# Optimization experiments

Measured on AMD Instinct MI355X. Metric: run time of the kernel, lower is better.

## Reference

```python
import jax, jax.numpy as jnp
import numpy as np
from jax import lax

NPOINT = 1024
NSAMPLE = 32
EPS = 1e-5


def setup_inputs() -> dict:
    key = jax.random.key(0)
    ks = jax.random.split(key, 8)
    B, N, CF = 16, 4096, 64
    xyz = jax.random.normal(ks[0], (B, N, 3), jnp.float32)
    points = jax.random.normal(ks[1], (B, N, CF), jnp.float32)
    in_ch = 3 + CF
    # 1x1 Conv2d weights stored as (out_ch, in_ch); kaiming-ish scale
    w0 = jax.random.normal(ks[2], (64, in_ch), jnp.float32) / np.sqrt(in_ch)
    w1 = jax.random.normal(ks[3], (64, 64), jnp.float32) / np.sqrt(64)
    w2 = jax.random.normal(ks[4], (128, 64), jnp.float32) / np.sqrt(64)
    z64 = jnp.zeros((64,), jnp.float32)
    z128 = jnp.zeros((128,), jnp.float32)
    o64 = jnp.ones((64,), jnp.float32)
    o128 = jnp.ones((128,), jnp.float32)
    return {
        "xyz": xyz, "points": points,
        "w0": w0, "b0": z64, "g0": o64, "bb0": z64,
        "w1": w1, "b1": z64, "g1": o64, "bb1": z64,
        "w2": w2, "b2": z128, "g2": o128, "bb2": z128,
    }


def _fps(xyz, npoint):
    """Iterative farthest point sampling. xyz: (B,N,3) -> (B,npoint) int32.
    Deterministic start at index 0 (torch uses a random start)."""
    B, N, _ = xyz.shape

    def step(carry, _):
        distance, farthest = carry
        centroid = jnp.take_along_axis(xyz, farthest[:, None, None], axis=1)  # (B,1,3)
        dist = jnp.sum((xyz - centroid) ** 2, -1)  # (B,N)
        distance = jnp.minimum(distance, dist)
        new_far = jnp.argmax(distance, axis=-1).astype(jnp.int32)
        return (distance, new_far), farthest

    init = (jnp.full((B, N), 1e10, xyz.dtype), jnp.zeros((B,), jnp.int32))
    _, cents = lax.scan(step, init, None, length=npoint)  # (npoint, B)
    return cents.T  # (B, npoint)


def _gather(pts, idx):
    """pts: (B,N,C), idx: (B,S,K) -> (B,S,K,C)"""
    return jax.vmap(lambda p, i: p[i])(pts, idx)


def _bn_relu(x, g, b):
    # training-mode BatchNorm over all axes except channel (last), biased var
    mean = jnp.mean(x, axis=(0, 1, 2))
    var = jnp.var(x, axis=(0, 1, 2))
    return jax.nn.relu(g * (x - mean) * lax.rsqrt(var + EPS) + b)


def reference(xyz, points, w0, b0, g0, bb0, w1, b1, g1, bb1, w2, b2, g2, bb2):
    B, N, _ = xyz.shape
    fps_idx = _fps(xyz, NPOINT)  # (B,S)
    new_xyz = jnp.take_along_axis(xyz, fps_idx[..., None], axis=1)  # (B,S,3)
    # squared distances centroid->all points: (B,S,N)
    d2 = (jnp.sum(new_xyz ** 2, -1)[:, :, None]
          + jnp.sum(xyz ** 2, -1)[:, None, :]
          - 2.0 * jnp.einsum("bsc,bnc->bsn", new_xyz, xyz))
    _, idx = lax.top_k(-d2, NSAMPLE)  # (B,S,K) nearest-K (sort-based ball query)
    grouped_xyz = _gather(xyz, idx) - new_xyz[:, :, None, :]  # (B,S,K,3)
    grouped_pts = _gather(points, idx)  # (B,S,K,CF)
    h = jnp.concatenate([grouped_xyz, grouped_pts], axis=-1)  # (B,S,K,3+CF)
    for w, b, g, bb in ((w0, b0, g0, bb0), (w1, b1, g1, bb1), (w2, b2, g2, bb2)):
        h = _bn_relu(jnp.einsum("bskc,oc->bsko", h, w) + b, g, bb)
    new_points = jnp.max(h, axis=2)  # (B,S,C_out) max over K
    new_points = jnp.transpose(new_points, (0, 2, 1))  # (B,C_out,S) matches torch
    return new_xyz, new_points
```

## Files before the change

### kernel.cpp

```cpp
#include <hip/hip_runtime.h>
#include <hip/hip_bf16.h>

#define NB 16
#define NN 4096
#define NS 1024
#define NK 32
#define CF 64
#define CIN 67
#define MTOT 524288
#define NEWP_OFF 49152

__device__ inline void stY(float* p, float v) { *p = v; }
__device__ inline void stY(__hip_bfloat16* p, float v) { *p = __float2bfloat16(v); }
__device__ inline float ldY(const float* p) { return *p; }
__device__ inline float ldY(const __hip_bfloat16* p) { return __bfloat162float(*p); }
__device__ inline float4 ldY4(const float* p) { return *(const float4*)p; }
__device__ inline float4 ldY4(const __hip_bfloat16* p) {
    return make_float4(ldY(p), ldY(p + 1), ldY(p + 2), ldY(p + 3));
}
__device__ inline void stY4(float* p, float4 v) { *(float4*)p = v; }
__device__ inline void stY4(__hip_bfloat16* p, float4 v) {
    stY(p, v.x); stY(p + 1, v.y); stY(p + 2, v.z); stY(p + 3, v.w);
}

template <int CTRL>
__device__ inline float dppredmax(float v) {
    int j = __builtin_amdgcn_update_dpp(__float_as_int(v), __float_as_int(v),
                                        CTRL, 0xF, 0xF, false);
    return fmaxf(v, __int_as_float(j));
}
template <int CTRL>
__device__ inline float dppredmin(float v) {
    int j = __builtin_amdgcn_update_dpp(__float_as_int(v), __float_as_int(v),
                                        CTRL, 0xF, 0xF, false);
    return fminf(v, __int_as_float(j));
}
template <int CTRL>
__device__ inline float dppadd0(float v) {
    int j = __builtin_amdgcn_update_dpp(0, __float_as_int(v), CTRL, 0xF, 0xF, true);
    return __fadd_rn(v, __int_as_float(j));
}
template <int CTRL>
__device__ inline unsigned long long dppredmin64(unsigned long long v) {
    int lo = (int)(unsigned)(v & 0xffffffffULL), hi = (int)(unsigned)(v >> 32);
    unsigned nlo = (unsigned)__builtin_amdgcn_update_dpp(lo, lo, CTRL, 0xF, 0xF, false);
    unsigned nhi = (unsigned)__builtin_amdgcn_update_dpp(hi, hi, CTRL, 0xF, 0xF, false);
    unsigned long long o = ((unsigned long long)nhi << 32) | nlo;
    return o < v ? o : v;
}
__device__ inline float wavemax_to_all(float tmax) {
    float g = tmax;
    g = dppredmax<0x111>(g);
    g = dppredmax<0x112>(g);
    g = dppredmax<0x114>(g);
    g = dppredmax<0x118>(g);
    g = dppredmax<0x142>(g);
    g = dppredmax<0x143>(g);
    return __int_as_float(__builtin_amdgcn_readlane(__float_as_int(g), 63));
}
__device__ inline unsigned long long wavemin64_to_all(unsigned long long v) {
    v = dppredmin64<0x111>(v);
    v = dppredmin64<0x112>(v);
    v = dppredmin64<0x114>(v);
    v = dppredmin64<0x118>(v);
    v = dppredmin64<0x142>(v);
    v = dppredmin64<0x143>(v);
    unsigned lo = (unsigned)__builtin_amdgcn_readlane((int)(unsigned)(v & 0xffffffffULL), 63);
    unsigned hi = (unsigned)__builtin_amdgcn_readlane((int)(unsigned)(v >> 32), 63);
    return ((unsigned long long)hi << 32) | lo;
}
__device__ inline float segsum16(float v) {
    v = dppadd0<0x111>(v); v = dppadd0<0x112>(v);
    v = dppadd0<0x114>(v); v = dppadd0<0x118>(v);
    return v;
}
__device__ inline float segsum32(float v) {
    v = segsum16(v); v = dppadd0<0x142>(v);
    return v;
}
__device__ inline float quadmax(float v) {
    v = dppredmax<0xB1>(v); v = dppredmax<0x4E>(v);
    return v;
}
__device__ inline float quadmin(float v) {
    v = dppredmin<0xB1>(v); v = dppredmin<0x4E>(v);
    return v;
}

__global__ __launch_bounds__(256) void fps_kernel(const float* __restrict__ xyz,
                                                  int* __restrict__ fps_idx) {
    __shared__ float4 cpt[NN];
    __shared__ unsigned long long part[2][4];
    const int b = blockIdx.x, t = threadIdx.x;
    const float4* src = (const float4*)(xyz + (size_t)b * NN * 3);
    float px[16], py[16], pz[16], dist[16];
#pragma unroll
    for (int j = 0; j < 4; ++j) {
        float4 A = src[t * 12 + 3 * j], B4 = src[t * 12 + 3 * j + 1], C4 = src[t * 12 + 3 * j + 2];
        px[4 * j + 0] = A.x;  py[4 * j + 0] = A.y;  pz[4 * j + 0] = A.z;
        px[4 * j + 1] = A.w;  py[4 * j + 1] = B4.x; pz[4 * j + 1] = B4.y;
        px[4 * j + 2] = B4.z; py[4 * j + 2] = B4.w; pz[4 * j + 2] = C4.x;
        px[4 * j + 3] = C4.y; py[4 * j + 3] = C4.z; pz[4 * j + 3] = C4.w;
    }
#pragma unroll
    for (int i = 0; i < 16; ++i) {
        dist[i] = 1e10f;
        cpt[16 * t + i] = make_float4(px[i], py[i], pz[i], 0.f);
    }
    __syncthreads();
    int cur = 0;
    float4 c = cpt[0];
    const int wv = t >> 6;
    for (int s = 0; s < NS; ++s) {
        if (t == 0) fps_idx[(b << 10) + s] = cur;
#pragma unroll
        for (int i = 0; i < 16; ++i) {
            float dx = __fsub_rn(px[i], c.x), dy = __fsub_rn(py[i], c.y), dz = __fsub_rn(pz[i], c.z);
            float d = __fadd_rn(__fadd_rn(__fmul_rn(dx, dx), __fmul_rn(dy, dy)), __fmul_rn(dz, dz));
            dist[i] = fminf(dist[i], d);
        }
        float m0 = fmaxf(dist[0], dist[1]),   m1 = fmaxf(dist[2], dist[3]);
        float m2 = fmaxf(dist[4], dist[5]),   m3 = fmaxf(dist[6], dist[7]);
        float m4 = fmaxf(dist[8], dist[9]),   m5 = fmaxf(dist[10], dist[11]);
        float m6 = fmaxf(dist[12], dist[13]), m7 = fmaxf(dist[14], dist[15]);
        m0 = fmaxf(m0, m1); m2 = fmaxf(m2, m3); m4 = fmaxf(m4, m5); m6 = fmaxf(m6, m7);
        m0 = fmaxf(m0, m2); m4 = fmaxf(m4, m6);
        const float tmax = fmaxf(m0, m4);
        int mi = 15;
#pragma unroll
        for (int i = 14; i >= 0; --i) mi = (dist[i] == tmax) ? i : mi;
        const float gmax = wavemax_to_all(tmax);
        unsigned long long mask = __ballot(tmax == gmax);
        int ldr = __ffsll(mask) - 1;
        int widx = __builtin_amdgcn_readlane(16 * t + mi, ldr);
        if ((t & 63) == 0) {
            part[s & 1][wv] =
                ((unsigned long long)__float_as_uint(gmax) << 32) | (unsigned)(4095 - widx);
        }
        __syncthreads();
        unsigned long long k0 = part[s & 1][0], k1 = part[s & 1][1];
        unsigned long long k2 = part[s & 1][2], k3 = part[s & 1][3];
        unsigned long long ka = k0 > k1 ? k0 : k1, kb = k2 > k3 ? k2 : k3;
        unsigned long long k = ka > kb ? ka : kb;
        cur = 4095 - (int)(unsigned)(k & 0xffffffffu);
        c = cpt[cur];
    }
}

__global__ __launch_bounds__(256) void knn_kernel(const float* __restrict__ xyz,
                                                  const int* __restrict__ fps_idx,
                                                  int* __restrict__ knn,
                                                  float* __restrict__ out) {
    __shared__ float4 cpt[NN];
    const int b = blockIdx.x >> 5, cb = blockIdx.x & 31, t = threadIdx.x;
    for (int p = t; p < NN; p += 256) {
        const float* xr = xyz + ((size_t)(b << 12) + p) * 3;
        float x = xr[0], y = xr[1], z = xr[2];
        float pn = __fadd_rn(__fadd_rn(__fmul_rn(x, x), __fmul_rn(y, y)), __fmul_rn(z, z));
        cpt[p] = make_float4(x, y, z, pn);
    }
    __syncthreads();
    const int lane = t & 63, wv = t >> 6;
    for (int r = 0; r < 8; ++r) {
        const int s = (cb << 5) + (wv << 3) + r;
        const int ci = fps_idx[(b << 10) + s];
        const float4 cq = cpt[ci];
        const float cx = cq.x, cy = cq.y, cz = cq.z, cn = cq.w;
        if (lane < 3) out[((size_t)(b << 10) + s) * 3 + lane] = (lane == 0) ? cx : (lane == 1 ? cy : cz);
        unsigned long long m1 = ~0ULL, m2 = ~0ULL, m3 = ~0ULL;
#pragma unroll
        for (int i = 0; i < 64; ++i) {
            int p = lane + (i << 6);
            float4 q = cpt[p];
            float dot = __fadd_rn(__fadd_rn(__fmul_rn(cx, q.x), __fmul_rn(cy, q.y)),
                                  __fmul_rn(cz, q.z));
            float d2 = __fsub_rn(__fadd_rn(cn, q.w), __fmul_rn(2.0f, dot));
            unsigned u = __float_as_uint(d2);
            unsigned enc = u ^ ((unsigned)((int)u >> 31) | 0x80000000u);
            unsigned long long key = ((unsigned long long)enc << 32) | (unsigned)p;
            if (key < m3) {
                if (key < m1)      { m3 = m2; m2 = m1; m1 = key; }
                else if (key < m2) { m3 = m2; m2 = key; }
                else               { m3 = key; }
            }
        }
        unsigned myidx = 0;
        for (int j = 0; j < 32; ++j) {
            const unsigned long long vmin = wavemin64_to_all(m1);
            if (lane == j) myidx = (unsigned)(vmin & 0xffffffffu);
            if (m1 == vmin) {
                m1 = m2; m2 = m3; m3 = ~0ULL;
                if (m1 == ~0ULL) {
#pragma unroll
                    for (int i = 0; i < 64; ++i) {
                        int p = lane + (i << 6);
                        float4 q = cpt[p];
                        float dot = __fadd_rn(__fadd_rn(__fmul_rn(cx, q.x), __fmul_rn(cy, q.y)),
                                              __fmul_rn(cz, q.z));
                        float d2 = __fsub_rn(__fadd_rn(cn, q.w), __fmul_rn(2.0f, dot));
                        unsigned u = __float_as_uint(d2);
                        unsigned enc = u ^ ((unsigned)((int)u >> 31) | 0x80000000u);
                        unsigned long long key = ((unsigned long long)enc << 32) | (unsigned)p;
                        if (key > vmin && key < m3) {
                            if (key < m1)      { m3 = m2; m2 = m1; m1 = key; }
                            else if (key < m2) { m3 = m2; m2 = key; }
                            else               { m3 = key; }
                        }
                    }
                }
            }
        }
        const int rowbase = ((b << 10) + s) << 5;
        if (lane < 32) knn[rowbase + lane] = (int)myidx;
    }
}

template <typename YT>
__global__ __launch_bounds__(256) void conv0_kernel(
    const float* __restrict__ xyz, const float* __restrict__ points,
    const float* __restrict__ out_xyz, const int* __restrict__ knn,
    const float* __restrict__ w0, const float* __restrict__ b0,
    YT* __restrict__ Y0, float* __restrict__ gs, float* __restrict__ gq) {
    __shared__ float Ht[CIN][128];
    __shared__ float Wt[CIN][64];
    __shared__ float bsm[64], bqm[64];
    const int t = threadIdx.x;
    const int eb = blockIdx.x << 7;
    for (int i = t; i < CIN * 64; i += 256) {
        int c = i >> 6, o = i & 63;
        Wt[c][o] = w0[o * CIN + c];
    }
    {
        const int le = t >> 1, part = t & 1;
        const int e = eb + le;
        const int b = e >> 15, s = (e >> 5) & 1023;
        const int pidx = knn[e];
        const float4* pr = (const float4*)(points + (((size_t)(b << 12) + pidx) << 6)) + (part << 3);
        if (part == 0) {
            const float* xr = xyz + ((size_t)(b << 12) + pidx) * 3;
            const float* cr = out_xyz + ((size_t)(b << 10) + s) * 3;
            Ht[0][le] = xr[0] - cr[0];
            Ht[1][le] = xr[1] - cr[1];
            Ht[2][le] = xr[2] - cr[2];
        }
#pragma unroll
        for (int q = 0; q < 8; ++q) {
            float4 v = pr[q];
            int c = 3 + (part << 5) + (q << 2);
            Ht[c][le] = v.x; Ht[c + 1][le] = v.y; Ht[c + 2][le] = v.z; Ht[c + 3][le] = v.w;
        }
    }
    __syncthreads();
    const int te = t & 31, to = t >> 5;
    float acc[4][8];
#pragma unroll
    for (int j = 0; j < 4; ++j)
#pragma unroll
        for (int i = 0; i < 8; ++i) acc[j][i] = 0.f;
#pragma unroll 2
    for (int c = 0; c < CIN; ++c) {
        const float4 a0 = *(const float4*)&Ht[c][te << 2];
        const float4 wa = *(const float4*)&Wt[c][to << 3];
        const float4 wb = *(const float4*)&Wt[c][(to << 3) + 4];
        const float av[4] = {a0.x, a0.y, a0.z, a0.w};
        const float wvv[8] = {wa.x, wa.y, wa.z, wa.w, wb.x, wb.y, wb.z, wb.w};
#pragma unroll
        for (int j = 0; j < 4; ++j)
#pragma unroll
            for (int i = 0; i < 8; ++i) acc[j][i] += av[j] * wvv[i];
    }
    const int o0 = to << 3;
    float s1v[8], s2v[8];
#pragma unroll
    for (int i = 0; i < 8; ++i) {
        const float bi = b0[o0 + i];
        float ss = 0.f, qq = 0.f;
#pragma unroll
        for (int j = 0; j < 4; ++j) {
            float v = acc[j][i] + bi;
            acc[j][i] = v;
            ss += v; qq += v * v;
        }
        s1v[i] = ss; s2v[i] = qq;
    }
#pragma unroll
    for (int i = 0; i < 8; ++i) {
        const size_t base = (size_t)(o0 + i) * MTOT + eb + (te << 2);
        stY4(&Y0[base], make_float4(acc[0][i], acc[1][i], acc[2][i], acc[3][i]));
    }
#pragma unroll
    for (int i = 0; i < 8; ++i) { s1v[i] = segsum32(s1v[i]); s2v[i] = segsum32(s2v[i]); }
    if ((t & 31) == 31) {
#pragma unroll
        for (int i = 0; i < 8; ++i) { bsm[o0 + i] = s1v[i]; bqm[o0 + i] = s2v[i]; }
    }
    __syncthreads();
    if (t < 64) atomicAdd(&gs[t], bsm[t]);
    else if (t < 128) atomicAdd(&gq[t - 64], bqm[t - 64]);
}

template <typename YT>
__global__ __launch_bounds__(256) void conv1_kernel(
    const YT* __restrict__ Y0, const float* __restrict__ w1, const float* __restrict__ b1,
    const float* __restrict__ sc, const float* __restrict__ sh,
    YT* __restrict__ Y1, float* __restrict__ gs, float* __restrict__ gq) {
    __shared__ float At[64][128];
    __shared__ float Wt[64][64];
    __shared__ float bsm[64], bqm[64];
    const int t = threadIdx.x;
    const int eb = blockIdx.x << 7;
    for (int i = t; i < 4096; i += 256) {
        int c = i >> 6, o = i & 63;
        Wt[c][o] = w1[o * 64 + c];
    }
#pragma unroll
    for (int r = 0; r < 8; ++r) {
        int L = (r << 8) + t;
        int c = L >> 5, col = (L & 31) << 2;
        float4 y = ldY4(&Y0[(size_t)c * MTOT + eb + col]);
        float sx = sc[c], hx = sh[c];
        At[c][col]     = fmaxf(sx * y.x + hx, 0.f);
        At[c][col + 1] = fmaxf(sx * y.y + hx, 0.f);
        At[c][col + 2] = fmaxf(sx * y.z + hx, 0.f);
        At[c][col + 3] = fmaxf(sx * y.w + hx, 0.f);
    }
    __syncthreads();
    const int te = t & 15, to = t >> 4;
    float acc[8][4];
#pragma unroll
    for (int j = 0; j < 8; ++j)
#pragma unroll
        for (int i = 0; i < 4; ++i) acc[j][i] = 0.f;
#pragma unroll 2
    for (int c = 0; c < 64; ++c) {
        const float4 a0 = *(const float4*)&At[c][te << 3];
        const float4 a1 = *(const float4*)&At[c][(te << 3) + 4];
        const float4 wa = *(const float4*)&Wt[c][to << 2];
        const float av[8] = {a0.x, a0.y, a0.z, a0.w, a1.x, a1.y, a1.z, a1.w};
        const float wvv[4] = {wa.x, wa.y, wa.z, wa.w};
#pragma unroll
        for (int j = 0; j < 8; ++j)
#pragma unroll
            for (int i = 0; i < 4; ++i) acc[j][i] += av[j] * wvv[i];
    }
    const int o0 = to << 2;
    float s1v[4], s2v[4];
#pragma unroll
    for (int i = 0; i < 4; ++i) {
        const float bi = b1[o0 + i];
        float ss = 0.f, qq = 0.f;
#pragma unroll
        for (int j = 0; j < 8; ++j) {
            float v = acc[j][i] + bi;
            acc[j][i] = v;
            ss += v; qq += v * v;
        }
        s1v[i] = ss; s2v[i] = qq;
    }
#pragma unroll
    for (int i = 0; i < 4; ++i) {
        const size_t base = (size_t)(o0 + i) * MTOT + eb + (te << 3);
        stY4(&Y1[base],     make_float4(acc[0][i], acc[1][i], acc[2][i], acc[3][i]));
        stY4(&Y1[base + 4], make_float4(acc[4][i], acc[5][i], acc[6][i], acc[7][i]));
    }
#pragma unroll
    for (int i = 0; i < 4; ++i) { s1v[i] = segsum16(s1v[i]); s2v[i] = segsum16(s2v[i]); }
    if ((t & 15) == 15) {
#pragma unroll
        for (int i = 0; i < 4; ++i) { bsm[o0 + i] = s1v[i]; bqm[o0 + i] = s2v[i]; }
    }
    __syncthreads();
    if (t < 64) atomicAdd(&gs[t], bsm[t]);
    else if (t < 128) atomicAdd(&gq[t - 64], bqm[t - 64]);
}

template <typename YT>
__global__ __launch_bounds__(256) void conv2s_kernel(
    const YT* __restrict__ Y1, const float* __restrict__ w2, const float* __restrict__ b2,
    const float* __restrict__ sc, const float* __restrict__ sh,
    float* __restrict__ gs, float* __restrict__ gq,
    float* __restrict__ Mx, float* __restrict__ Mn) {
    __shared__ float At[64][128];
    __shared__ float Wt[64][128];
    __shared__ float bsm[128], bqm[128];
    __shared__ float mxs[4][128], mns[4][128];
    const int t = threadIdx.x;
    const int eb = blockIdx.x << 7;
    for (int i = t; i < 8192; i += 256) {
        int o = i & 127, c = i >> 7;
        Wt[c][o] = w2[o * 64 + c];
    }
#pragma unroll
    for (int r = 0; r < 8; ++r) {
        int L = (r << 8) + t;
        int c = L >> 5, col = (L & 31) << 2;
        float4 y = ldY4(&Y1[(size_t)c * MTOT + eb + col]);
        float sx = sc[c], hx = sh[c];
        At[c][col]     = fmaxf(sx * y.x + hx, 0.f);
        At[c][col + 1] = fmaxf(sx * y.y + hx, 0.f);
        At[c][col + 2] = fmaxf(sx * y.z + hx, 0.f);
        At[c][col + 3] = fmaxf(sx * y.w + hx, 0.f);
    }
    __syncthreads();
    const int te = t & 15, to = t >> 4;
    float acc[8][8];
#pragma unroll
    for (int j = 0; j < 8; ++j)
#pragma unroll
        for (int i = 0; i < 8; ++i) acc[j][i] = 0.f;
#pragma unroll 2
    for (int c = 0; c < 64; ++c) {
        const float4 a0 = *(const float4*)&At[c][te << 3];
        const float4 a1 = *(const float4*)&At[c][(te << 3) + 4];
        const float4 wa = *(const float4*)&Wt[c][to << 3];
        const float4 wb = *(const float4*)&Wt[c][(to << 3) + 4];
        const float av[8] = {a0.x, a0.y, a0.z, a0.w, a1.x, a1.y, a1.z, a1.w};
        const float wvv[8] = {wa.x, wa.y, wa.z, wa.w, wb.x, wb.y, wb.z, wb.w};
#pragma unroll
        for (int j = 0; j < 8; ++j)
#pragma unroll
            for (int i = 0; i < 8; ++i) acc[j][i] += av[j] * wvv[i];
    }
    const int o0 = to << 3;
    float s1v[8], s2v[8], mxv[8], mnv[8];
#pragma unroll
    for (int i = 0; i < 8; ++i) {
        const float bi = b2[o0 + i];
        float ss = 0.f, qq = 0.f;
        float mx = -3.4e38f, mn = 3.4e38f;
#pragma unroll
        for (int j = 0; j < 8; ++j) {
            float v = acc[j][i] + bi;
            ss += v; qq += v * v;
            mx = fmaxf(mx, v); mn = fminf(mn, v);
        }
        s1v[i] = ss; s2v[i] = qq; mxv[i] = mx; mnv[i] = mn;
    }
#pragma unroll
    for (int i = 0; i < 8; ++i) {
        s1v[i] = segsum16(s1v[i]); s2v[i] = segsum16(s2v[i]);
        mxv[i] = quadmax(mxv[i]);  mnv[i] = quadmin(mnv[i]);
    }
    if ((t & 15) == 15) {
#pragma unroll
        for (int i = 0; i < 8; ++i) { bsm[o0 + i] = s1v[i]; bqm[o0 + i] = s2v[i]; }
    }
    if ((t & 3) == 0) {
        const int srow = (t & 15) >> 2;
#pragma unroll
        for (int i = 0; i < 8; ++i) { mxs[srow][o0 + i] = mxv[i]; mns[srow][o0 + i] = mnv[i]; }
    }
    __syncthreads();
    if (t < 128) atomicAdd(&gs[t], bsm[t]);
    else atomicAdd(&gq[t - 128], bqm[t - 128]);
    const int sidx0 = blockIdx.x << 2;
    for (int i = t; i < 512; i += 256) {
        int row = i >> 7, o = i & 127;
        Mx[(size_t)(sidx0 + row) * 128 + o] = mxs[row][o];
        Mn[(size_t)(sidx0 + row) * 128 + o] = mns[row][o];
    }
}

__global__ __launch_bounds__(256) void final2_kernel(
    const float* __restrict__ Mx, const float* __restrict__ Mn,
    const float* __restrict__ sc2, const float* __restrict__ sh2,
    float* __restrict__ out) {
    __shared__ float T[128][65];
    const int t = threadIdx.x;
    const int b = blockIdx.x >> 4, s0 = (blockIdx.x & 15) << 6;
    for (int i = t; i < 8192; i += 256) {
        int r = i >> 7, o = i & 127;
        size_t src = ((size_t)(b << 10) + s0 + r) * 128 + o;
        float a = sc2[o];
        float m = (a >= 0.f) ? Mx[src] : Mn[src];
        T[o][r] = fmaxf(a * m + sh2[o], 0.f);
    }
    __syncthreads();
    float* np = out + NEWP_OFF;
    for (int i = t; i < 8192; i += 256) {
        int o = i >> 6, r = i & 63;
        np[((size_t)(b << 7) + o) * 1024 + s0 + r] = T[o][r];
    }
}

__global__ void fin_kernel(const float* __restrict__ gs, const float* __restrict__ gq,
                           const float* __restrict__ g, const float* __restrict__ bb,
                           float* __restrict__ sc, float* __restrict__ sh, int C) {
    const int o = threadIdx.x;
    if (o < C) {
        const float inv = 1.f / (float)MTOT;
        float mean = gs[o] * inv;
        float var = gq[o] * inv - mean * mean;
        float r = g[o] / sqrtf(var + 1e-5f);
        sc[o] = r;
        sh[o] = bb[o] - mean * r;
    }
}

extern "C" void kernel_launch(void* const* d_in, const int* in_sizes, int n_in,
                              void* d_out, int out_size, void* d_ws, size_t ws_size,
                              hipStream_t stream) {
    const float* xyz = (const float*)d_in[0];
    const float* points = (const float*)d_in[1];
    const float* w0 = (const float*)d_in[2];
    const float* b0 = (const float*)d_in[3];
    const float* g0 = (const float*)d_in[4];
    const float* bb0 = (const float*)d_in[5];
    const float* w1 = (const float*)d_in[6];
    const float* b1 = (const float*)d_in[7];
    const float* g1 = (const float*)d_in[8];
    const float* bb1 = (const float*)d_in[9];
    const float* w2 = (const float*)d_in[10];
    const float* b2 = (const float*)d_in[11];
    const float* g2 = (const float*)d_in[12];
    const float* bb2 = (const float*)d_in[13];
    float* out = (float*)d_out;
    char* ws = (char*)d_ws;

    int* knn = (int*)(ws);
    int* fps = (int*)(ws + (2u << 20));
    float* stats = (float*)(ws + (2u << 20) + (1u << 16));
    float* bn = stats + 512;
    float *gs0 = stats, *gq0 = stats + 64, *gs1 = stats + 128, *gq1 = stats + 192;
    float *gs2 = stats + 256, *gq2 = stats + 384;
    float *sc0 = bn, *sh0 = bn + 64, *sc1 = bn + 128, *sh1 = bn + 192;
    float *sc2 = bn + 256, *sh2 = bn + 384;
    float* Mx = (float*)(ws + (4ull << 20));
    float* Mn = (float*)(ws + (12ull << 20));
    const size_t yoff = 20ull << 20;
    const size_t ybytes_f32 = (size_t)MTOT * 64 * 4;
    const bool f32p = ws_size >= yoff + 2 * ybytes_f32;

    (void)hipMemsetAsync(stats, 0, 512 * sizeof(float), stream);
    fps_kernel<<<NB, 256, 0, stream>>>(xyz, fps);
    knn_kernel<<<NB * 32, 256, 0, stream>>>(xyz, fps, knn, out);

    if (f32p) {
        float* Y0 = (float*)(ws + yoff);
        float* Y1 = Y0 + (size_t)MTOT * 64;
        conv0_kernel<float><<<4096, 256, 0, stream>>>(xyz, points, out, knn, w0, b0, Y0, gs0, gq0);
        fin_kernel<<<1, 64, 0, stream>>>(gs0, gq0, g0, bb0, sc0, sh0, 64);
        conv1_kernel<float><<<4096, 256, 0, stream>>>(Y0, w1, b1, sc0, sh0, Y1, gs1, gq1);
        fin_kernel<<<1, 64, 0, stream>>>(gs1, gq1, g1, bb1, sc1, sh1, 64);
        conv2s_kernel<float><<<4096, 256, 0, stream>>>(Y1, w2, b2, sc1, sh1, gs2, gq2, Mx, Mn);
        fin_kernel<<<1, 128, 0, stream>>>(gs2, gq2, g2, bb2, sc2, sh2, 128);
    } else {
        __hip_bfloat16* Y0 = (__hip_bfloat16*)(ws + yoff);
        __hip_bfloat16* Y1 = Y0 + (size_t)MTOT * 64;
        conv0_kernel<__hip_bfloat16><<<4096, 256, 0, stream>>>(xyz, points, out, knn, w0, b0, Y0, gs0, gq0);
        fin_kernel<<<1, 64, 0, stream>>>(gs0, gq0, g0, bb0, sc0, sh0, 64);
        conv1_kernel<__hip_bfloat16><<<4096, 256, 0, stream>>>(Y0, w1, b1, sc0, sh0, Y1, gs1, gq1);
        fin_kernel<<<1, 64, 0, stream>>>(gs1, gq1, g1, bb1, sc1, sh1, 64);
        conv2s_kernel<__hip_bfloat16><<<4096, 256, 0, stream>>>(Y1, w2, b2, sc1, sh1, gs2, gq2, Mx, Mn);
        fin_kernel<<<1, 128, 0, stream>>>(gs2, gq2, g2, bb2, sc2, sh2, 128);
    }
    final2_kernel<<<256, 256, 0, stream>>>(Mx, Mn, sc2, sh2, out);
}
```

Measured before the change: 1.289 ms.

## Carry FPS centroid coords through reduction and fold BN finalize into consumers

The FPS loop no longer stages all points in LDS. Each wave leader writes its candidate's coordinates next to the max distance and index, so the next centroid comes straight from the cross-wave reduction instead of an LDS lookup by index. Separately, the three tiny fin_kernel launches are removed, and each consumer kernel recomputes the BatchNorm scale and shift from the accumulated sums in its prologue. This cuts kernel launches and a dependent LDS load on the serial FPS critical path. In exchange every block repeats a small amount of redundant math, and ties are now broken through a float-encoded index comparison.

```diff
diff --git a/kernel.cpp b/kernel.cpp
--- a/kernel.cpp
+++ b/kernel.cpp
@@ -89,8 +89,8 @@
 
 __global__ __launch_bounds__(256) void fps_kernel(const float* __restrict__ xyz,
                                                   int* __restrict__ fps_idx) {
-    __shared__ float4 cpt[NN];
-    __shared__ unsigned long long part[2][4];
+    __shared__ float4 partA[2][4];
+    __shared__ __align__(16) float partZ[2][4];
     const int b = blockIdx.x, t = threadIdx.x;
     const float4* src = (const float4*)(xyz + (size_t)b * NN * 3);
     float px[16], py[16], pz[16], dist[16];
@@ -103,19 +103,16 @@
         px[4 * j + 3] = C4.y; py[4 * j + 3] = C4.z; pz[4 * j + 3] = C4.w;
     }
 #pragma unroll
-    for (int i = 0; i < 16; ++i) {
-        dist[i] = 1e10f;
-        cpt[16 * t + i] = make_float4(px[i], py[i], pz[i], 0.f);
-    }
-    __syncthreads();
+    for (int i = 0; i < 16; ++i) dist[i] = 1e10f;
     int cur = 0;
-    float4 c = cpt[0];
-    const int wv = t >> 6;
+    const float* p0 = xyz + (size_t)b * NN * 3;
+    float cx = p0[0], cy = p0[1], cz = p0[2];
+    const int lane = t & 63, wv = t >> 6;
     for (int s = 0; s < NS; ++s) {
         if (t == 0) fps_idx[(b << 10) + s] = cur;
 #pragma unroll
         for (int i = 0; i < 16; ++i) {
-            float dx = __fsub_rn(px[i], c.x), dy = __fsub_rn(py[i], c.y), dz = __fsub_rn(pz[i], c.z);
+            float dx = __fsub_rn(px[i], cx), dy = __fsub_rn(py[i], cy), dz = __fsub_rn(pz[i], cz);
             float d = __fadd_rn(__fadd_rn(__fmul_rn(dx, dx), __fmul_rn(dy, dy)), __fmul_rn(dz, dz));
             dist[i] = fminf(dist[i], d);
         }
@@ -127,23 +124,32 @@
         m0 = fmaxf(m0, m2); m4 = fmaxf(m4, m6);
         const float tmax = fmaxf(m0, m4);
         int mi = 15;
-#pragma unroll
-        for (int i = 14; i >= 0; --i) mi = (dist[i] == tmax) ? i : mi;
+        float sx = px[15], sy = py[15], sz = pz[15];
+#pragma unroll
+        for (int i = 14; i >= 0; --i) {
+            bool hit = (dist[i] == tmax);
+            mi = hit ? i : mi;
+            sx = hit ? px[i] : sx; sy = hit ? py[i] : sy; sz = hit ? pz[i] : sz;
+        }
         const float gmax = wavemax_to_all(tmax);
         unsigned long long mask = __ballot(tmax == gmax);
         int ldr = __ffsll(mask) - 1;
-        int widx = __builtin_amdgcn_readlane(16 * t + mi, ldr);
-        if ((t & 63) == 0) {
-            part[s & 1][wv] =
-                ((unsigned long long)__float_as_uint(gmax) << 32) | (unsigned)(4095 - widx);
+        if (lane == ldr) {
+            partA[s & 1][wv] = make_float4(gmax, (float)(4095 - (16 * t + mi)), sx, sy);
+            partZ[s & 1][wv] = sz;
         }
         __syncthreads();
-        unsigned long long k0 = part[s & 1][0], k1 = part[s & 1][1];
-        unsigned long long k2 = part[s & 1][2], k3 = part[s & 1][3];
-        unsigned long long ka = k0 > k1 ? k0 : k1, kb = k2 > k3 ? k2 : k3;
-        unsigned long long k = ka > kb ? ka : kb;
-        cur = 4095 - (int)(unsigned)(k & 0xffffffffu);
-        c = cpt[cur];
+        float4 A0 = partA[s & 1][0], A1 = partA[s & 1][1];
+        float4 A2 = partA[s & 1][2], A3 = partA[s & 1][3];
+        float4 Z = *(const float4*)&partZ[s & 1][0];
+        bool c1 = (A1.x > A0.x) || (A1.x == A0.x && A1.y > A0.y);
+        float4 B0 = c1 ? A1 : A0; float z0 = c1 ? Z.y : Z.x;
+        bool c2 = (A3.x > A2.x) || (A3.x == A2.x && A3.y > A2.y);
+        float4 B1 = c2 ? A3 : A2; float z1 = c2 ? Z.w : Z.z;
+        bool c3 = (B1.x > B0.x) || (B1.x == B0.x && B1.y > B0.y);
+        float4 W = c3 ? B1 : B0;
+        cur = 4095 - (int)W.y;
+        cx = W.z; cy = W.w; cz = c3 ? z1 : z0;
     }
 }
 
@@ -302,23 +308,33 @@
 template <typename YT>
 __global__ __launch_bounds__(256) void conv1_kernel(
     const YT* __restrict__ Y0, const float* __restrict__ w1, const float* __restrict__ b1,
-    const float* __restrict__ sc, const float* __restrict__ sh,
+    const float* __restrict__ gsp, const float* __restrict__ gqp,
+    const float* __restrict__ g, const float* __restrict__ bb,
     YT* __restrict__ Y1, float* __restrict__ gs, float* __restrict__ gq) {
     __shared__ float At[64][128];
     __shared__ float Wt[64][64];
+    __shared__ float bnsc[64], bnsh[64];
     __shared__ float bsm[64], bqm[64];
     const int t = threadIdx.x;
     const int eb = blockIdx.x << 7;
+    if (t < 64) {
+        const float inv = 1.f / (float)MTOT;
+        float mean = gsp[t] * inv;
+        float var = gqp[t] * inv - mean * mean;
+        float r = g[t] / sqrtf(var + 1e-5f);
+        bnsc[t] = r; bnsh[t] = bb[t] - mean * r;
+    }
     for (int i = t; i < 4096; i += 256) {
         int c = i >> 6, o = i & 63;
         Wt[c][o] = w1[o * 64 + c];
     }
+    __syncthreads();
 #pragma unroll
     for (int r = 0; r < 8; ++r) {
         int L = (r << 8) + t;
         int c = L >> 5, col = (L & 31) << 2;
         float4 y = ldY4(&Y0[(size_t)c * MTOT + eb + col]);
-        float sx = sc[c], hx = sh[c];
+        float sx = bnsc[c], hx = bnsh[c];
         At[c][col]     = fmaxf(sx * y.x + hx, 0.f);
         At[c][col + 1] = fmaxf(sx * y.y + hx, 0.f);
         At[c][col + 2] = fmaxf(sx * y.z + hx, 0.f);
@@ -377,25 +393,35 @@
 template <typename YT>
 __global__ __launch_bounds__(256) void conv2s_kernel(
     const YT* __restrict__ Y1, const float* __restrict__ w2, const float* __restrict__ b2,
-    const float* __restrict__ sc, const float* __restrict__ sh,
+    const float* __restrict__ gsp, const float* __restrict__ gqp,
+    const float* __restrict__ g, const float* __restrict__ bb,
     float* __restrict__ gs, float* __restrict__ gq,
     float* __restrict__ Mx, float* __restrict__ Mn) {
     __shared__ float At[64][128];
     __shared__ float Wt[64][128];
+    __shared__ float bnsc[64], bnsh[64];
     __shared__ float bsm[128], bqm[128];
     __shared__ float mxs[4][128], mns[4][128];
     const int t = threadIdx.x;
     const int eb = blockIdx.x << 7;
+    if (t < 64) {
+        const float inv = 1.f / (float)MTOT;
+        float mean = gsp[t] * inv;
+        float var = gqp[t] * inv - mean * mean;
+        float r = g[t] / sqrtf(var + 1e-5f);
+        bnsc[t] = r; bnsh[t] = bb[t] - mean * r;
+    }
     for (int i = t; i < 8192; i += 256) {
         int o = i & 127, c = i >> 7;
         Wt[c][o] = w2[o * 64 + c];
     }
+    __syncthreads();
 #pragma unroll
     for (int r = 0; r < 8; ++r) {
         int L = (r << 8) + t;
         int c = L >> 5, col = (L & 31) << 2;
         float4 y = ldY4(&Y1[(size_t)c * MTOT + eb + col]);
-        float sx = sc[c], hx = sh[c];
+        float sx = bnsc[c], hx = bnsh[c];
         At[c][col]     = fmaxf(sx * y.x + hx, 0.f);
         At[c][col + 1] = fmaxf(sx * y.y + hx, 0.f);
         At[c][col + 2] = fmaxf(sx * y.z + hx, 0.f);
@@ -463,37 +489,33 @@
 
 __global__ __launch_bounds__(256) void final2_kernel(
     const float* __restrict__ Mx, const float* __restrict__ Mn,
-    const float* __restrict__ sc2, const float* __restrict__ sh2,
+    const float* __restrict__ gsp, const float* __restrict__ gqp,
+    const float* __restrict__ g, const float* __restrict__ bb,
     float* __restrict__ out) {
     __shared__ float T[128][65];
+    __shared__ float bnsc[128], bnsh[128];
     const int t = threadIdx.x;
+    if (t < 128) {
+        const float inv = 1.f / (float)MTOT;
+        float mean = gsp[t] * inv;
+        float var = gqp[t] * inv - mean * mean;
+        float r = g[t] / sqrtf(var + 1e-5f);
+        bnsc[t] = r; bnsh[t] = bb[t] - mean * r;
+    }
+    __syncthreads();
     const int b = blockIdx.x >> 4, s0 = (blockIdx.x & 15) << 6;
     for (int i = t; i < 8192; i += 256) {
         int r = i >> 7, o = i & 127;
         size_t src = ((size_t)(b << 10) + s0 + r) * 128 + o;
-        float a = sc2[o];
+        float a = bnsc[o];
         float m = (a >= 0.f) ? Mx[src] : Mn[src];
-        T[o][r] = fmaxf(a * m + sh2[o], 0.f);
+        T[o][r] = fmaxf(a * m + bnsh[o], 0.f);
     }
     __syncthreads();
     float* np = out + NEWP_OFF;
     for (int i = t; i < 8192; i += 256) {
         int o = i >> 6, r = i & 63;
         np[((size_t)(b << 7) + o) * 1024 + s0 + r] = T[o][r];
-    }
-}
-
-__global__ void fin_kernel(const float* __restrict__ gs, const float* __restrict__ gq,
-                           const float* __restrict__ g, const float* __restrict__ bb,
-                           float* __restrict__ sc, float* __restrict__ sh, int C) {
-    const int o = threadIdx.x;
-    if (o < C) {
-        const float inv = 1.f / (float)MTOT;
-        float mean = gs[o] * inv;
-        float var = gq[o] * inv - mean * mean;
-        float r = g[o] / sqrtf(var + 1e-5f);
-        sc[o] = r;
-        sh[o] = bb[o] - mean * r;
     }
 }
 
@@ -520,11 +542,8 @@
     int* knn = (int*)(ws);
     int* fps = (int*)(ws + (2u << 20));
     float* stats = (float*)(ws + (2u << 20) + (1u << 16));
-    float* bn = stats + 512;
     float *gs0 = stats, *gq0 = stats + 64, *gs1 = stats + 128, *gq1 = stats + 192;
     float *gs2 = stats + 256, *gq2 = stats + 384;
-    float *sc0 = bn, *sh0 = bn + 64, *sc1 = bn + 128, *sh1 = bn + 192;
-    float *sc2 = bn + 256, *sh2 = bn + 384;
     float* Mx = (float*)(ws + (4ull << 20));
     float* Mn = (float*)(ws + (12ull << 20));
     const size_t yoff = 20ull << 20;
@@ -539,20 +558,14 @@
         float* Y0 = (float*)(ws + yoff);
         float* Y1 = Y0 + (size_t)MTOT * 64;
         conv0_kernel<float><<<4096, 256, 0, stream>>>(xyz, points, out, knn, w0, b0, Y0, gs0, gq0);
-        fin_kernel<<<1, 64, 0, stream>>>(gs0, gq0, g0, bb0, sc0, sh0, 64);
-        conv1_kernel<float><<<4096, 256, 0, stream>>>(Y0, w1, b1, sc0, sh0, Y1, gs1, gq1);
-        fin_kernel<<<1, 64, 0, stream>>>(gs1, gq1, g1, bb1, sc1, sh1, 64);
-        conv2s_kernel<float><<<4096, 256, 0, stream>>>(Y1, w2, b2, sc1, sh1, gs2, gq2, Mx, Mn);
-        fin_kernel<<<1, 128, 0, stream>>>(gs2, gq2, g2, bb2, sc2, sh2, 128);
+        conv1_kernel<float><<<4096, 256, 0, stream>>>(Y0, w1, b1, gs0, gq0, g0, bb0, Y1, gs1, gq1);
+        conv2s_kernel<float><<<4096, 256, 0, stream>>>(Y1, w2, b2, gs1, gq1, g1, bb1, gs2, gq2, Mx, Mn);
     } else {
         __hip_bfloat16* Y0 = (__hip_bfloat16*)(ws + yoff);
         __hip_bfloat16* Y1 = Y0 + (size_t)MTOT * 64;
         conv0_kernel<__hip_bfloat16><<<4096, 256, 0, stream>>>(xyz, points, out, knn, w0, b0, Y0, gs0, gq0);
-        fin_kernel<<<1, 64, 0, stream>>>(gs0, gq0, g0, bb0, sc0, sh0, 64);
-        conv1_kernel<__hip_bfloat16><<<4096, 256, 0, stream>>>(Y0, w1, b1, sc0, sh0, Y1, gs1, gq1);
-        fin_kernel<<<1, 64, 0, stream>>>(gs1, gq1, g1, bb1, sc1, sh1, 64);
-        conv2s_kernel<__hip_bfloat16><<<4096, 256, 0, stream>>>(Y1, w2, b2, sc1, sh1, gs2, gq2, Mx, Mn);
-        fin_kernel<<<1, 128, 0, stream>>>(gs2, gq2, g2, bb2, sc2, sh2, 128);
-    }
-    final2_kernel<<<256, 256, 0, stream>>>(Mx, Mn, sc2, sh2, out);
-}
+        conv1_kernel<__hip_bfloat16><<<4096, 256, 0, stream>>>(Y0, w1, b1, gs0, gq0, g0, bb0, Y1, gs1, gq1);
+        conv2s_kernel<__hip_bfloat16><<<4096, 256, 0, stream>>>(Y1, w2, b2, gs1, gq1, g1, bb1, gs2, gq2, Mx, Mn);
+    }
+    final2_kernel<<<256, 256, 0, stream>>>(Mx, Mn, gs2, gq2, g2, bb2, out);
+}
```

Result: slower. 1.708 ms (+32.4%).
